# Kernel optimization log

Hardware: AMD Instinct MI355X
Metric: run time of the kernel (lower is better)

Reference implementation:

```python
import jax, jax.numpy as jnp
import numpy as np

B, N, H, K, WIN = 512, 600, 256, 9, 129
AVG = 1.5
PAD = K // 2
PWIN = WIN + 2 * PAD  # padded window length


def setup_inputs() -> dict:
    key = jax.random.key(0)
    ks = jax.random.split(key, 8)
    tokens = jax.random.normal(ks[0], (B, N, H), dtype=jnp.float32)
    token_keys = jax.random.normal(ks[1], (B, H, N), dtype=jnp.float32)
    query = jax.random.normal(ks[2], (B, H), dtype=jnp.float32)
    num_tokens = jax.random.randint(ks[3], (B,), 300, N + 1, dtype=jnp.int32)
    tokens_mask = jnp.arange(N)[None, :] < num_tokens[:, None]
    u = jax.random.uniform(ks[4], (B,))
    window_start = (u * (num_tokens - WIN + 1).astype(jnp.float32)).astype(jnp.int32)
    alignment = jax.random.uniform(ks[5], (B, N + 2 * PAD), dtype=jnp.float32)
    cum_alignment = jax.random.uniform(ks[6], (B, N + 2 * PAD), dtype=jnp.float32) * 50.0
    conv_w = jax.random.normal(ks[7], (H, 2, K), dtype=jnp.float32) * 0.1
    conv_b = jnp.zeros((H,), dtype=jnp.float32)
    return dict(tokens=tokens, tokens_mask=tokens_mask, token_keys=token_keys,
                num_tokens=num_tokens, query=query, alignment=alignment,
                cum_alignment=cum_alignment, window_start=window_start,
                conv_w=conv_w, conv_b=conv_b)


def reference(tokens, tokens_mask, token_keys, num_tokens, query, alignment,
              cum_alignment, window_start, conv_w, conv_b):
    scale = jnp.sqrt(jnp.float32(H))
    idx = window_start[:, None] + jnp.arange(WIN)
    pidx = window_start[:, None] + jnp.arange(PWIN)        # [B, PWIN]
    mask_w = jnp.take_along_axis(tokens_mask, idx, axis=1)
    tokens_w = jnp.take_along_axis(tokens, idx[:, :, None], axis=1)
    keys_w = jnp.take_along_axis(token_keys, idx[:, None, :], axis=2)
    last_w = jnp.take_along_axis(alignment, pidx, axis=1)                  # [B, PWIN]
    cum_w = jnp.take_along_axis(cum_alignment, pidx, axis=1)               # [B, PWIN]
    position = jnp.stack([cum_w / AVG - 1.0, last_w * 2.0 - 1.0], axis=1)  # [B, 2, PWIN]
    position = jax.lax.stop_gradient(position)  # .detach() in torch
    feat = jax.lax.conv_general_dilated(position, conv_w, (1,), 'VALID',
                                        dimension_numbers=('NCH', 'OIH', 'NCH'))
    feat = feat + conv_b[None, :, None]
    keys = feat + keys_w
    score = jnp.einsum('bh,bhw->bw', query, keys) / scale
    score = jnp.where(mask_w, score, -jnp.inf)
    align_w = jax.nn.softmax(score, axis=1)
    context = jnp.einsum('bw,bwh->bh', align_w, tokens_w)                  # [B, H]
    b_idx = jnp.arange(B)[:, None]
    full_align = jnp.zeros_like(alignment).at[b_idx, idx + PAD].set(align_w)
    new_start = jnp.argmax(full_align, axis=1).astype(jnp.int32) - PWIN // 2
    new_start = jnp.maximum(window_start, new_start)
    new_start = jnp.minimum(new_start, num_tokens - WIN)
    new_start = jnp.maximum(new_start, 0)
    unpadded = full_align[:, PAD:-PAD]                                     # [B, N]
    return (context, unpadded, full_align, cum_alignment + full_align, new_start)
```

## Files before the change

kernel.cpp:

```cpp
#include <hip/hip_runtime.h>
#include <math.h>

#define BB   512
#define NN   600
#define HH   256
#define KS   9
#define WIN  129
#define PADW 4
#define PWIN 137
#define NP   608

__global__ __launch_bounds__(512, 8) void attn_kernel(
    const float* __restrict__ tokens,
    const float* __restrict__ token_keys,
    const int*   __restrict__ num_tokens,
    const float* __restrict__ query,
    const float* __restrict__ alignment,
    const float* __restrict__ cum_align,
    const int*   __restrict__ window_start,
    const float* __restrict__ conv_w,
    const float* __restrict__ conv_b,
    float* __restrict__ out)
{
  const int b    = blockIdx.x;
  const int t    = threadIdx.x;
  const int lane = t & 63;
  const int wv   = t >> 6;

  __shared__ float sq[HH];
  __shared__ float p0[PWIN], p1[PWIN];
  __shared__ float cred[19][8];
  __shared__ float w128red[4];
  __shared__ float sqc[19];
  __shared__ float sS[8][130];
  __shared__ float salign[WIN];
  __shared__ __align__(16) float sctx[8][HH];
  __shared__ float s_sum;
  __shared__ int   s_arg;

  const int ws = window_start[b];
  const int nt = num_tokens[b];
  const float* __restrict__ Kb = token_keys + (size_t)b * (HH * NN);

  const float cum0 = cum_align[b * NP + t];
  const float cum1 = (t + 512 < NP) ? cum_align[b * NP + t + 512] : 0.f;

  float qreg = 0.f;
  if (t < HH) { qreg = query[b * HH + t]; sq[t] = qreg; }
  if (t < PWIN) {
    p0[t] = cum_align[b * NP + ws + t] * (1.0f / 1.5f) - 1.0f;
    p1[t] = alignment[b * NP + ws + t] * 2.0f - 1.0f;
  }
  __syncthreads();

  {
    const float* __restrict__ Kp  = Kb + (size_t)(wv * 32) * NN + ws;
    const float* __restrict__ sqp = sq + wv * 32;
    float a0 = 0.f, a1 = 0.f;
    #pragma unroll 4
    for (int h = 0; h < 32; ++h) {
      const float q = sqp[h];
      a0 += q * Kp[(size_t)h * NN + lane];
      a1 += q * Kp[(size_t)h * NN + 64 + lane];
    }
    sS[wv][lane]      = a0;
    sS[wv][64 + lane] = a1;
  }

  if (t < HH) {
    float v = qreg * Kb[(size_t)t * NN + ws + 128];
    #pragma unroll
    for (int off = 32; off; off >>= 1) v += __shfl_xor(v, off, 64);
    if (lane == 0) w128red[wv] = v;
  }

  if (t < 152) {
    const int j = t >> 3, seg = t & 7;
    const int h0 = seg * 32;
    float a = 0.f;
    if (j < 18) {
      #pragma unroll 4
      for (int h = 0; h < 32; ++h) a += sq[h0 + h] * conv_w[(h0 + h) * 18 + j];
    } else {
      #pragma unroll 4
      for (int h = 0; h < 32; ++h) a += sq[h0 + h] * conv_b[h0 + h];
    }
    cred[j][seg] = a;
  }
  __syncthreads();

  if (t < 19) {
    const float* c = cred[t];
    sqc[t] = ((c[0] + c[1]) + (c[2] + c[3])) + ((c[4] + c[5]) + (c[6] + c[7]));
  }
  __syncthreads();

  if (t < WIN) {
    float dot;
    if (t < 128) {
      dot = 0.f;
      #pragma unroll
      for (int g = 0; g < 8; ++g) dot += sS[g][t];
    } else {
      dot = w128red[0] + w128red[1] + w128red[2] + w128red[3];
    }
    float f = sqc[18];
    #pragma unroll
    for (int k = 0; k < KS; ++k) f += sqc[k] * p0[t + k] + sqc[9 + k] * p1[t + k];
    float sc = (dot + f) * 0.0625f;
    if (ws + t >= nt) sc = -INFINITY;
    salign[t] = sc;
  }
  __syncthreads();

  if (t < 64) {
    const float a0 = salign[t];
    const float a1 = salign[t + 64];
    const float a2 = (t == 0) ? salign[128] : -INFINITY;
    float m = a0; int idx = t;
    if (a1 > m) { m = a1; idx = t + 64; }
    if (a2 > m) { m = a2; idx = 128; }
    #pragma unroll
    for (int off = 32; off; off >>= 1) {
      const float om = __shfl_xor(m, off, 64);
      const int   oi = __shfl_xor(idx, off, 64);
      if (om > m || (om == m && oi < idx)) { m = om; idx = oi; }
    }
    const float e0 = expf(a0 - m);
    const float e1 = expf(a1 - m);
    salign[t]      = e0;
    salign[t + 64] = e1;
    float s = e0 + e1;
    if (t == 0) { const float e2 = expf(a2 - m); salign[128] = e2; s += e2; }
    #pragma unroll
    for (int off = 32; off; off >>= 1) s += __shfl_xor(s, off, 64);
    if (t == 0) { s_sum = s; s_arg = idx; }
  }
  __syncthreads();

  const float inv = 1.0f / s_sum;

  float* out0 = out;
  float* out1 = out0 + BB * HH;
  float* out2 = out1 + BB * NN;
  float* out3 = out2 + BB * NP;
  float* out4 = out3 + BB * NP;

  {
    const float* __restrict__ Tb = tokens + (size_t)b * (NN * HH) + (size_t)ws * HH;
    float4 acc = make_float4(0.f, 0.f, 0.f, 0.f);
    #pragma unroll 4
    for (int i = 0; i < 16; ++i) {
      const int w = wv + 8 * i;
      const float a = salign[w];
      const float4 v4 = ((const float4*)(Tb + (size_t)w * HH))[lane];
      acc.x += a * v4.x; acc.y += a * v4.y; acc.z += a * v4.z; acc.w += a * v4.w;
    }
    if (wv == 0) {
      const float a = salign[128];
      const float4 v4 = ((const float4*)(Tb + (size_t)128 * HH))[lane];
      acc.x += a * v4.x; acc.y += a * v4.y; acc.z += a * v4.z; acc.w += a * v4.w;
    }
    ((float4*)&sctx[wv][0])[lane] = acc;
  }

  for (int j = t; j < NN; j += 512) {
    const float v = (j >= ws && j <= ws + 128) ? salign[j - ws] * inv : 0.f;
    out1[b * NN + j] = v;
  }
  {
    int j = t;
    const float v0 = (j >= ws + PADW && j <= ws + PADW + 128) ? salign[j - ws - PADW] * inv : 0.f;
    out2[b * NP + j] = v0;
    out3[b * NP + j] = v0 + cum0;
    j = t + 512;
    if (j < NP) {
      const float v1 = (j >= ws + PADW && j <= ws + PADW + 128) ? salign[j - ws - PADW] * inv : 0.f;
      out2[b * NP + j] = v1;
      out3[b * NP + j] = v1 + cum1;
    }
  }
  if (t == 0) {
    int jstar = ws + PADW + s_arg;
    int ns = jstar - (PWIN / 2);
    ns = max(ws, ns);
    ns = min(ns, nt - WIN);
    ns = max(ns, 0);
    out4[b] = (float)ns;
  }
  __syncthreads();

  if (t < HH) {
    float c = 0.f;
    #pragma unroll
    for (int v = 0; v < 8; ++v) c += sctx[v][t];
    out0[b * HH + t] = c * inv;
  }
}

extern "C" void kernel_launch(void* const* d_in, const int* in_sizes, int n_in,
                              void* d_out, int out_size, void* d_ws, size_t ws_size,
                              hipStream_t stream) {
  const float* tokens       = (const float*)d_in[0];
  const float* token_keys   = (const float*)d_in[2];
  const int*   num_tokens   = (const int*)d_in[3];
  const float* query        = (const float*)d_in[4];
  const float* alignment    = (const float*)d_in[5];
  const float* cum_align    = (const float*)d_in[6];
  const int*   window_start = (const int*)d_in[7];
  const float* conv_w       = (const float*)d_in[8];
  const float* conv_b       = (const float*)d_in[9];

  attn_kernel<<<BB, 512, 0, stream>>>(tokens, token_keys, num_tokens, query,
                                      alignment, cum_align, window_start,
                                      conv_w, conv_b, (float*)d_out);
}
```

Before: 515.0 us.

## Prefetch token window into registers early and double block size to 1024 threads

The block grows from 512 to 1024 threads (16 waves). Each wave now loads its slice of the 129-row token window into registers at kernel start, so those global loads overlap with the key dot products, conv and softmax instead of being issued after the softmax. The key dot product is split across twice as many waves, and the output stores no longer need a loop. The cost is higher register pressure from nine float4 values held across the kernel, and fewer resident blocks per CU at the larger block size.

Measured after the change: 517.7 us. About the same (+0.5%).

```diff
diff --git a/kernel.cpp b/kernel.cpp
--- a/kernel.cpp
+++ b/kernel.cpp
@@ -10,7 +10,7 @@
 #define PWIN 137
 #define NP   608
 
-__global__ __launch_bounds__(512, 8) void attn_kernel(
+__global__ __launch_bounds__(1024) void attn_kernel(
     const float* __restrict__ tokens,
     const float* __restrict__ token_keys,
     const int*   __restrict__ num_tokens,
@@ -34,16 +34,31 @@
   __shared__ float sqc[19];
   __shared__ float sS[8][130];
   __shared__ float salign[WIN];
-  __shared__ __align__(16) float sctx[8][HH];
+  __shared__ __align__(16) float sctx[16][HH];
   __shared__ float s_sum;
   __shared__ int   s_arg;
 
   const int ws = window_start[b];
   const int nt = num_tokens[b];
   const float* __restrict__ Kb = token_keys + (size_t)b * (HH * NN);
-
-  const float cum0 = cum_align[b * NP + t];
-  const float cum1 = (t + 512 < NP) ? cum_align[b * NP + t + 512] : 0.f;
+  const float* __restrict__ Tb = tokens + (size_t)b * (NN * HH) + (size_t)ws * HH;
+
+  float4 r0, r1, r2, r3, r4, r5, r6, r7;
+  {
+    const float4* T4 = (const float4*)Tb;
+    r0 = T4[(size_t)(wv +   0) * 64 + lane];
+    r1 = T4[(size_t)(wv +  16) * 64 + lane];
+    r2 = T4[(size_t)(wv +  32) * 64 + lane];
+    r3 = T4[(size_t)(wv +  48) * 64 + lane];
+    r4 = T4[(size_t)(wv +  64) * 64 + lane];
+    r5 = T4[(size_t)(wv +  80) * 64 + lane];
+    r6 = T4[(size_t)(wv +  96) * 64 + lane];
+    r7 = T4[(size_t)(wv + 112) * 64 + lane];
+  }
+  float4 r8 = make_float4(0.f, 0.f, 0.f, 0.f);
+  if (wv == 0) r8 = ((const float4*)Tb)[(size_t)128 * 64 + lane];
+
+  const float cum0 = (t < NP) ? cum_align[b * NP + t] : 0.f;
 
   float qreg = 0.f;
   if (t < HH) { qreg = query[b * HH + t]; sq[t] = qreg; }
@@ -54,17 +69,15 @@
   __syncthreads();
 
   {
-    const float* __restrict__ Kp  = Kb + (size_t)(wv * 32) * NN + ws;
-    const float* __restrict__ sqp = sq + wv * 32;
-    float a0 = 0.f, a1 = 0.f;
-    #pragma unroll 4
-    for (int h = 0; h < 32; ++h) {
-      const float q = sqp[h];
-      a0 += q * Kp[(size_t)h * NN + lane];
-      a1 += q * Kp[(size_t)h * NN + 64 + lane];
-    }
-    sS[wv][lane]      = a0;
-    sS[wv][64 + lane] = a1;
+    const int hh   = wv & 7;
+    const int wseg = wv >> 3;
+    const int w    = wseg * 64 + lane;
+    const float* __restrict__ Kp  = Kb + (size_t)(hh * 32) * NN + ws + w;
+    const float* __restrict__ sqp = sq + hh * 32;
+    float acc = 0.f;
+    #pragma unroll 8
+    for (int h = 0; h < 32; ++h) acc += sqp[h] * Kp[(size_t)h * NN];
+    sS[hh][w] = acc;
   }
 
   if (t < HH) {
@@ -147,38 +160,30 @@
   float* out4 = out3 + BB * NP;
 
   {
-    const float* __restrict__ Tb = tokens + (size_t)b * (NN * HH) + (size_t)ws * HH;
-    float4 acc = make_float4(0.f, 0.f, 0.f, 0.f);
-    #pragma unroll 4
-    for (int i = 0; i < 16; ++i) {
-      const int w = wv + 8 * i;
-      const float a = salign[w];
-      const float4 v4 = ((const float4*)(Tb + (size_t)w * HH))[lane];
-      acc.x += a * v4.x; acc.y += a * v4.y; acc.z += a * v4.z; acc.w += a * v4.w;
-    }
+    float4 acc;
+    float a;
+    a = salign[wv +   0]; acc.x  = a * r0.x; acc.y  = a * r0.y; acc.z  = a * r0.z; acc.w  = a * r0.w;
+    a = salign[wv +  16]; acc.x += a * r1.x; acc.y += a * r1.y; acc.z += a * r1.z; acc.w += a * r1.w;
+    a = salign[wv +  32]; acc.x += a * r2.x; acc.y += a * r2.y; acc.z += a * r2.z; acc.w += a * r2.w;
+    a = salign[wv +  48]; acc.x += a * r3.x; acc.y += a * r3.y; acc.z += a * r3.z; acc.w += a * r3.w;
+    a = salign[wv +  64]; acc.x += a * r4.x; acc.y += a * r4.y; acc.z += a * r4.z; acc.w += a * r4.w;
+    a = salign[wv +  80]; acc.x += a * r5.x; acc.y += a * r5.y; acc.z += a * r5.z; acc.w += a * r5.w;
+    a = salign[wv +  96]; acc.x += a * r6.x; acc.y += a * r6.y; acc.z += a * r6.z; acc.w += a * r6.w;
+    a = salign[wv + 112]; acc.x += a * r7.x; acc.y += a * r7.y; acc.z += a * r7.z; acc.w += a * r7.w;
     if (wv == 0) {
-      const float a = salign[128];
-      const float4 v4 = ((const float4*)(Tb + (size_t)128 * HH))[lane];
-      acc.x += a * v4.x; acc.y += a * v4.y; acc.z += a * v4.z; acc.w += a * v4.w;
+      a = salign[128];    acc.x += a * r8.x; acc.y += a * r8.y; acc.z += a * r8.z; acc.w += a * r8.w;
     }
     ((float4*)&sctx[wv][0])[lane] = acc;
   }
 
-  for (int j = t; j < NN; j += 512) {
-    const float v = (j >= ws && j <= ws + 128) ? salign[j - ws] * inv : 0.f;
-    out1[b * NN + j] = v;
-  }
-  {
-    int j = t;
-    const float v0 = (j >= ws + PADW && j <= ws + PADW + 128) ? salign[j - ws - PADW] * inv : 0.f;
-    out2[b * NP + j] = v0;
-    out3[b * NP + j] = v0 + cum0;
-    j = t + 512;
-    if (j < NP) {
-      const float v1 = (j >= ws + PADW && j <= ws + PADW + 128) ? salign[j - ws - PADW] * inv : 0.f;
-      out2[b * NP + j] = v1;
-      out3[b * NP + j] = v1 + cum1;
-    }
+  if (t < NN) {
+    const float v = (t >= ws && t <= ws + 128) ? salign[t - ws] * inv : 0.f;
+    out1[b * NN + t] = v;
+  }
+  if (t < NP) {
+    const float v = (t >= ws + PADW && t <= ws + PADW + 128) ? salign[t - ws - PADW] * inv : 0.f;
+    out2[b * NP + t] = v;
+    out3[b * NP + t] = v + cum0;
   }
   if (t == 0) {
     int jstar = ws + PADW + s_arg;
@@ -193,7 +198,7 @@
   if (t < HH) {
     float c = 0.f;
     #pragma unroll
-    for (int v = 0; v < 8; ++v) c += sctx[v][t];
+    for (int v = 0; v < 16; ++v) c += sctx[v][t];
     out0[b * HH + t] = c * inv;
   }
 }
@@ -211,7 +216,7 @@
   const float* conv_w       = (const float*)d_in[8];
   const float* conv_b       = (const float*)d_in[9];
 
-  attn_kernel<<<BB, 512, 0, stream>>>(tokens, token_keys, num_tokens, query,
-                                      alignment, cum_align, window_start,
-                                      conv_w, conv_b, (float*)d_out);
+  attn_kernel<<<BB, 1024, 0, stream>>>(tokens, token_keys, num_tokens, query,
+                                       alignment, cum_align, window_start,
+                                       conv_w, conv_b, (float*)d_out);
 }
```
